# Performance work log

Measured on AMD Instinct MI355X. Metric: run time of the kernel, lower is better.

## Reference

```python
import jax, jax.numpy as jnp
import numpy as np

R = 0.15          # ball-query radius (module init arg r)
K = 32            # _MAX_NEIGHBOURS
B, N = 8, 4096


def _ball_query(pos, r, k):
    """Dense ball query. pos: [B,N,3] -> neighbor idx [B,N,K], sorted by distance.
    Slots with fewer than k in-radius neighbors are filled with the query's own
    index (self is always the first neighbor at distance 0), so their
    contribution to (f_i - f_j)^2 is exactly 0 -- matching torch-points-kernels'
    fill-with-first-neighbor behaviour."""
    d2 = jnp.sum((pos[:, :, None, :] - pos[:, None, :, :]) ** 2, axis=-1)  # [B,N,N]
    masked = jnp.where(d2 <= r * r, d2, jnp.inf)
    neg_vals, idx = jax.lax.top_k(-masked, k)          # ascending distance
    valid = neg_vals > -jnp.inf
    self_idx = jnp.arange(pos.shape[1])[None, :, None]
    return jnp.where(valid, idx, self_idx)             # [B,N,K]


def setup_inputs() -> dict:
    key = jax.random.key(0)
    k1, k2 = jax.random.split(key)
    pos = jax.random.uniform(k1, (B, N, 3), dtype=jnp.float32)
    f = jax.random.normal(k2, (B, N), dtype=jnp.float32)
    return {"pos": pos, "f": f}


def reference(pos, f):
    # neighbor indices are non-differentiable (torch gathers with long indices)
    nei_idx = jax.lax.stop_gradient(_ball_query(pos, R, K))      # [B,N,K]
    f_nei = jax.vmap(lambda fb, ib: fb[ib])(f, nei_idx)          # [B,N,K]
    variances = jnp.sum((f[:, :, None] - f_nei) ** 2, axis=-1)   # [B,N]
    return 0.5 * jnp.mean(variances)
```

## Files before the change

### kernel.cpp

```cpp
#include <hip/hip_runtime.h>


#define BQ_K 32
#define CAP 128
#define WPB 4
#define G 6
#define NC (G * G * G)
#define CAPC 512
#define QMAX 64
#define NPTS 4096
#define NPART 64
#define PSTRIDE 16

__device__ __forceinline__ int cell_coord(float x) {
    int c = (int)(x * (float)G);
    return c < 0 ? 0 : (c > G - 1 ? G - 1 : c);
}

__device__ __forceinline__ unsigned int decode_cnt(unsigned int v) {
    return (v >= 0x80000000u) ? (v - 0xAAAAAAAAu) : v;
}

__device__ __forceinline__ float select_sum(float2 e0, float2 e1, int M,
                                            float r2) {
    if (M <= BQ_K) return e0.y + e1.y;
    float lo = 0.0f, hi = r2 * 1.000001f;
    #pragma unroll
    for (int it = 0; it < 12; ++it) {
        const float mid = 0.5f * (lo + hi);
        const int cnt = __popcll(__ballot(e0.x < mid)) +
                        __popcll(__ballot(e1.x < mid));
        if (cnt >= BQ_K) hi = mid; else lo = mid;
    }
    float s = 0.0f;
    if (e0.x < hi) s = e0.y;
    if (e1.x < hi) s += e1.y;
    return s;
}

__device__ __forceinline__ float dual_select_sum(
    float2 a0, float2 a1, int MA, float2 b0, float2 b1, int MB, float r2)
{
    const bool needA = MA > BQ_K;
    const bool needB = MB > BQ_K;
    float hiA = 1e31f, hiB = 1e31f;
    if (needA || needB) {
        float loA = 0.0f, loB = 0.0f;
        if (needA) hiA = r2 * 1.000001f;
        if (needB) hiB = r2 * 1.000001f;
        const bool bigA = MA > 64, bigB = MB > 64;
        #pragma unroll
        for (int it = 0; it < 12; ++it) {
            if (needA) {
                const float mid = 0.5f * (loA + hiA);
                int c = __popcll(__ballot(a0.x < mid));
                if (bigA) c += __popcll(__ballot(a1.x < mid));
                if (c >= BQ_K) hiA = mid; else loA = mid;
            }
            if (needB) {
                const float mid = 0.5f * (loB + hiB);
                int c = __popcll(__ballot(b0.x < mid));
                if (bigB) c += __popcll(__ballot(b1.x < mid));
                if (c >= BQ_K) hiB = mid; else loB = mid;
            }
        }
    }
    float s = 0.0f;
    if (a0.x < hiA) s += a0.y;
    if (a1.x < hiA) s += a1.y;
    if (b0.x < hiB) s += b0.y;
    if (b1.x < hiB) s += b1.y;
    return s;
}

__global__ __launch_bounds__(256) void dl_fused(
    const float* __restrict__ pos, const float* __restrict__ f,
    float* __restrict__ partial, unsigned int* __restrict__ c1,
    unsigned int* __restrict__ c2, float* __restrict__ out,
    float r2, float scale)
{
    __shared__ float4 s_cand[CAPC];
    __shared__ float2 s_sel[WPB][2][CAP];
    __shared__ int    s_q[QMAX];
    __shared__ int    s_ncand, s_nq;
    __shared__ float  s_wsum[WPB];
    __shared__ int    s_last;

    const int bc = blockIdx.x;
    const int b  = bc / NC;
    const int c  = bc - b * NC;
    const int cx = c % G, cy = (c / G) % G, cz = c / (G * G);

    const int lane = threadIdx.x & 63;
    const int wave = threadIdx.x >> 6;
    const unsigned long long lmask = (1ULL << lane) - 1ULL;

    if (threadIdx.x == 0) { s_ncand = 0; s_nq = 0; s_last = 0; }
    __syncthreads();

    const float* posb = pos + (size_t)b * NPTS * 3;
    const float* fb   = f   + (size_t)b * NPTS;

    const float lox = cx * (1.0f / G), hix = lox + (1.0f / G);
    const float loy = cy * (1.0f / G), hiy = loy + (1.0f / G);
    const float loz = cz * (1.0f / G), hiz = loz + (1.0f / G);

    constexpr int per = NPTS / WPB;
    const int wbeg = wave * per;
    for (int j0 = 0; j0 < per; j0 += 64) {
        const int j = wbeg + j0 + lane;
        const float x  = posb[3 * j + 0];
        const float y  = posb[3 * j + 1];
        const float z  = posb[3 * j + 2];
        const float fv = fb[j];
        const float ddx = fmaxf(fmaxf(lox - x, x - hix), 0.0f);
        const float ddy = fmaxf(fmaxf(loy - y, y - hiy), 0.0f);
        const float ddz = fmaxf(fmaxf(loz - z, z - hiz), 0.0f);
        const float d2c = fmaf(ddx, ddx, fmaf(ddy, ddy, ddz * ddz));
        const bool in = (d2c <= r2);
        const unsigned long long m = __ballot(in);
        const int nh = __popcll(m);
        int base = 0;
        if (lane == 0 && nh) base = atomicAdd(&s_ncand, nh);
        base = __shfl(base, 0, 64);
        if (in) {
            const int off = base + __popcll(m & lmask);
            if (off < CAPC) {
                s_cand[off] = make_float4(x, y, z, fv);
                if (cell_coord(x) == cx && cell_coord(y) == cy &&
                    cell_coord(z) == cz) {
                    const int qs = atomicAdd(&s_nq, 1);
                    if (qs < QMAX) s_q[qs] = off;
                }
            }
        }
    }
    __syncthreads();

    const int ncand = s_ncand < CAPC ? s_ncand : CAPC;
    const int nq    = s_nq < QMAX ? s_nq : QMAX;
    const int ncB   = (ncand + 63) & ~63;

    for (int i = ncand + threadIdx.x; i < ncB; i += 256)
        s_cand[i] = make_float4(1e30f, 1e30f, 1e30f, 0.0f);
    __syncthreads();

    float2* selA = s_sel[wave][0];
    float2* selB = s_sel[wave][1];
    float wsum = 0.0f;

    for (int qi = wave; qi < nq; qi += 2 * WPB) {
        const int  qj    = qi + WPB;
        const bool haveB = qj < nq;
        const float4 qpA = s_cand[s_q[qi]];
        const float4 qpB = s_cand[s_q[haveB ? qj : qi]];
        const float qxA = qpA.x, qyA = qpA.y, qzA = qpA.z, fiA = qpA.w;
        const float qxB = qpB.x, qyB = qpB.y, qzB = qpB.z, fiB = qpB.w;

        int cinA = 0, cinB = 0;
        for (int basej = 0; basej < ncB; basej += 64) {
            const float4 cd = s_cand[basej + lane];
            const float dxA = cd.x - qxA, dyA = cd.y - qyA, dzA = cd.z - qzA;
            const float dxB = cd.x - qxB, dyB = cd.y - qyB, dzB = cd.z - qzB;
            const float d2A = fmaf(dxA, dxA, fmaf(dyA, dyA, dzA * dzA));
            const float d2B = fmaf(dxB, dxB, fmaf(dyB, dyB, dzB * dzB));
            const bool inbA = d2A <= r2;
            const bool inbB = haveB && (d2B <= r2);
            const unsigned long long mA = __ballot(inbA);
            const unsigned long long mB = __ballot(inbB);
            const int offA = cinA + __popcll(mA & lmask);
            const int offB = cinB + __popcll(mB & lmask);
            if (inbA && offA < CAP) {
                const float fd = fiA - cd.w;
                selA[offA] = make_float2(d2A, fd * fd);
            }
            if (inbB && offB < CAP) {
                const float fd = fiB - cd.w;
                selB[offB] = make_float2(d2B, fd * fd);
            }
            cinA += __popcll(mA);
            cinB += __popcll(mB);
        }
        const int MA = cinA < CAP ? cinA : CAP;
        const int MB = cinB < CAP ? cinB : CAP;
        const float2 a0 = (lane < MA) ? selA[lane] : make_float2(1e30f, 0.0f);
        const float2 a1 = (64 + lane < MA) ? selA[64 + lane]
                                           : make_float2(1e30f, 0.0f);
        const float2 b0 = (lane < MB) ? selB[lane] : make_float2(1e30f, 0.0f);
        const float2 b1 = (64 + lane < MB) ? selB[64 + lane]
                                           : make_float2(1e30f, 0.0f);
        wsum += dual_select_sum(a0, a1, MA, b0, b1, MB, r2);
    }

    for (int o = 32; o > 0; o >>= 1) wsum += __shfl_down(wsum, o, 64);
    if (lane == 0) s_wsum[wave] = wsum;
    __syncthreads();
    if (threadIdx.x == 0) {
        const float bs = s_wsum[0] + s_wsum[1] + s_wsum[2] + s_wsum[3];
        const int k = blockIdx.x & (NPART - 1);
        const float oldp = atomicAdd(&partial[k * PSTRIDE], bs);
        asm volatile("" :: "v"(oldp));
        const unsigned int expect = (gridDim.x - 1u - (unsigned)k) / 64u + 1u;
        const unsigned int oc =
            decode_cnt(atomicAdd(&c1[k * PSTRIDE], 1u));
        if (oc + 1u == expect) {
            const unsigned int o2 = decode_cnt(atomicAdd(c2, 1u));
            if (o2 + 1u == (unsigned)NPART)
                s_last = 1;
        }
    }
    __syncthreads();
    if (s_last && wave == 0) {
        float v = atomicAdd(&partial[lane * PSTRIDE], 0.0f);
        for (int o = 32; o > 0; o >>= 1) v += __shfl_down(v, o, 64);
        if (lane == 0) out[0] = v * scale;
    }
}

__global__ __launch_bounds__(256) void dl_fallback(
    const float* __restrict__ pos, const float* __restrict__ f,
    float* __restrict__ out, float r2, float scale)
{
    __shared__ float4 s_cand[CAPC];
    __shared__ float2 s_sel[WPB][CAP];
    __shared__ int    s_q[QMAX];
    __shared__ int    s_ncand, s_nq;
    __shared__ float  s_wsum[WPB];

    const int bc = blockIdx.x;
    const int b  = bc / NC;
    const int c  = bc - b * NC;
    const int cx = c % G, cy = (c / G) % G, cz = c / (G * G);
    const int lane = threadIdx.x & 63;
    const int wave = threadIdx.x >> 6;
    const unsigned long long lmask = (1ULL << lane) - 1ULL;

    if (threadIdx.x == 0) { s_ncand = 0; s_nq = 0; }
    __syncthreads();

    const float* posb = pos + (size_t)b * NPTS * 3;
    const float* fb   = f   + (size_t)b * NPTS;
    const float lox = cx * (1.0f / G), hix = lox + (1.0f / G);
    const float loy = cy * (1.0f / G), hiy = loy + (1.0f / G);
    const float loz = cz * (1.0f / G), hiz = loz + (1.0f / G);

    constexpr int per = NPTS / WPB;
    const int wbeg = wave * per;
    for (int j0 = 0; j0 < per; j0 += 64) {
        const int j = wbeg + j0 + lane;
        const float x  = posb[3 * j + 0];
        const float y  = posb[3 * j + 1];
        const float z  = posb[3 * j + 2];
        const float ddx = fmaxf(fmaxf(lox - x, x - hix), 0.0f);
        const float ddy = fmaxf(fmaxf(loy - y, y - hiy), 0.0f);
        const float ddz = fmaxf(fmaxf(loz - z, z - hiz), 0.0f);
        const float d2c = fmaf(ddx, ddx, fmaf(ddy, ddy, ddz * ddz));
        const bool in = (d2c <= r2);
        const unsigned long long m = __ballot(in);
        const int nh = __popcll(m);
        int base = 0;
        if (lane == 0 && nh) base = atomicAdd(&s_ncand, nh);
        base = __shfl(base, 0, 64);
        if (in) {
            const int off = base + __popcll(m & lmask);
            if (off < CAPC) {
                s_cand[off] = make_float4(x, y, z, fb[j]);
                if (cell_coord(x) == cx && cell_coord(y) == cy &&
                    cell_coord(z) == cz) {
                    const int qs = atomicAdd(&s_nq, 1);
                    if (qs < QMAX) s_q[qs] = off;
                }
            }
        }
    }
    __syncthreads();

    const int ncand = s_ncand < CAPC ? s_ncand : CAPC;
    const int nq    = s_nq < QMAX ? s_nq : QMAX;
    const int ncB   = (ncand + 63) & ~63;
    float2* sel = s_sel[wave];
    float wsum = 0.0f;

    for (int qi = wave; qi < nq; qi += WPB) {
        const float4 qp = s_cand[s_q[qi]];
        const float qx = qp.x, qy = qp.y, qz = qp.z, fi = qp.w;
        int cin = 0;
        for (int basej = 0; basej < ncB; basej += 64) {
            const float4 cd = s_cand[basej + lane];
            const bool valid = (basej + lane) < ncand;
            const float dx = cd.x - qx, dy = cd.y - qy, dz = cd.z - qz;
            const float d2 = fmaf(dx, dx, fmaf(dy, dy, dz * dz));
            const bool inb = valid && (d2 <= r2);
            const unsigned long long mm = __ballot(inb);
            const int off = cin + __popcll(mm & lmask);
            if (inb && off < CAP) {
                const float fd = fi - cd.w;
                sel[off] = make_float2(d2, fd * fd);
            }
            cin += __popcll(mm);
        }
        const int M = cin < CAP ? cin : CAP;
        const float2 e0 = (lane < M) ? sel[lane] : make_float2(1e30f, 0.0f);
        const float2 e1 = (64 + lane < M) ? sel[64 + lane]
                                          : make_float2(1e30f, 0.0f);
        wsum += select_sum(e0, e1, M, r2);
    }

    for (int o = 32; o > 0; o >>= 1) wsum += __shfl_down(wsum, o, 64);
    if (lane == 0) s_wsum[wave] = wsum;
    __syncthreads();
    if (threadIdx.x == 0) {
        const float bs = s_wsum[0] + s_wsum[1] + s_wsum[2] + s_wsum[3];
        atomicAdd(out, bs * scale);
    }
}

extern "C" void kernel_launch(void* const* d_in, const int* in_sizes, int n_in,
                              void* d_out, int out_size, void* d_ws, size_t ws_size,
                              hipStream_t stream) {
    const float* pos = (const float*)d_in[0];
    const float* f   = (const float*)d_in[1];
    float* out = (float*)d_out;

    const int B = in_sizes[1] / NPTS;
    const int total = B * NPTS;
    const float r2 = 0.15f * 0.15f;
    const float scale = 0.5f / (float)total;

    const size_t part_bytes = (size_t)NPART * PSTRIDE * sizeof(float);
    const size_t c1_bytes   = (size_t)NPART * PSTRIDE * sizeof(unsigned);
    const size_t c2_bytes   = 64;
    if (ws_size < part_bytes + c1_bytes + c2_bytes) {
        hipMemsetAsync(out, 0, sizeof(float), stream);
        dl_fallback<<<B * NC, 256, 0, stream>>>(pos, f, out, r2, scale);
        return;
    }

    char* wsp = (char*)d_ws;
    float*        partial = (float*)wsp;
    unsigned int* c1      = (unsigned int*)(wsp + part_bytes);
    unsigned int* c2      = (unsigned int*)(wsp + part_bytes + c1_bytes);

    dl_fused<<<B * NC, 256, 0, stream>>>(pos, f, partial, c1, c2, out,
                                         r2, scale);
}
```

Baseline: 79.48 us.

## Process two adjacent x-cells per block to share the point scan

Each block now handles a pair of neighbouring grid cells along x, scanning all points of the batch once and building two candidate lists and query lists in shared memory. Waves are split two per cell for the distance/selection phase. This halves the number of blocks and the redundant global reads of the full point set per cell, at the cost of doubled shared memory for candidates and half the waves per cell's query work.

```diff
diff --git a/kernel.cpp b/kernel.cpp
--- a/kernel.cpp
+++ b/kernel.cpp
@@ -6,6 +6,7 @@
 #define WPB 4
 #define G 6
 #define NC (G * G * G)
+#define NPAIR (NC / 2)
 #define CAPC 512
 #define QMAX 64
 #define NPTS 4096
@@ -73,35 +74,38 @@
     return s;
 }
 
-__global__ __launch_bounds__(256) void dl_fused(
+__global__ __launch_bounds__(256) void dl_fused2(
     const float* __restrict__ pos, const float* __restrict__ f,
     float* __restrict__ partial, unsigned int* __restrict__ c1,
     unsigned int* __restrict__ c2, float* __restrict__ out,
     float r2, float scale)
 {
-    __shared__ float4 s_cand[CAPC];
+    __shared__ float4 s_cand[2][CAPC];
     __shared__ float2 s_sel[WPB][2][CAP];
-    __shared__ int    s_q[QMAX];
-    __shared__ int    s_ncand, s_nq;
+    __shared__ int    s_q[2][QMAX];
+    __shared__ int    s_nc0, s_nc1, s_nq0, s_nq1;
     __shared__ float  s_wsum[WPB];
     __shared__ int    s_last;
 
     const int bc = blockIdx.x;
-    const int b  = bc / NC;
-    const int c  = bc - b * NC;
-    const int cx = c % G, cy = (c / G) % G, cz = c / (G * G);
+    const int b  = bc / NPAIR;
+    const int pr = bc - b * NPAIR;
+    const int c0 = pr * 2;
+    const int cx0 = c0 % G, cy = (c0 / G) % G, cz = c0 / (G * G);
 
     const int lane = threadIdx.x & 63;
     const int wave = threadIdx.x >> 6;
     const unsigned long long lmask = (1ULL << lane) - 1ULL;
 
-    if (threadIdx.x == 0) { s_ncand = 0; s_nq = 0; s_last = 0; }
+    if (threadIdx.x == 0) { s_nc0 = 0; s_nc1 = 0; s_nq0 = 0; s_nq1 = 0;
+                            s_last = 0; }
     __syncthreads();
 
     const float* posb = pos + (size_t)b * NPTS * 3;
     const float* fb   = f   + (size_t)b * NPTS;
 
-    const float lox = cx * (1.0f / G), hix = lox + (1.0f / G);
+    const float lox0 = cx0 * (1.0f / G), hix0 = lox0 + (1.0f / G);
+    const float hix1 = hix0 + (1.0f / G);
     const float loy = cy * (1.0f / G), hiy = loy + (1.0f / G);
     const float loz = cz * (1.0f / G), hiz = loz + (1.0f / G);
 
@@ -113,53 +117,90 @@
         const float y  = posb[3 * j + 1];
         const float z  = posb[3 * j + 2];
         const float fv = fb[j];
-        const float ddx = fmaxf(fmaxf(lox - x, x - hix), 0.0f);
         const float ddy = fmaxf(fmaxf(loy - y, y - hiy), 0.0f);
         const float ddz = fmaxf(fmaxf(loz - z, z - hiz), 0.0f);
-        const float d2c = fmaf(ddx, ddx, fmaf(ddy, ddy, ddz * ddz));
-        const bool in = (d2c <= r2);
-        const unsigned long long m = __ballot(in);
-        const int nh = __popcll(m);
-        int base = 0;
-        if (lane == 0 && nh) base = atomicAdd(&s_ncand, nh);
-        base = __shfl(base, 0, 64);
-        if (in) {
-            const int off = base + __popcll(m & lmask);
-            if (off < CAPC) {
-                s_cand[off] = make_float4(x, y, z, fv);
-                if (cell_coord(x) == cx && cell_coord(y) == cy &&
-                    cell_coord(z) == cz) {
-                    const int qs = atomicAdd(&s_nq, 1);
-                    if (qs < QMAX) s_q[qs] = off;
+        const float dyz2 = fmaf(ddy, ddy, ddz * ddz);
+        const float ddx0 = fmaxf(fmaxf(lox0 - x, x - hix0), 0.0f);
+        const float ddx1 = fmaxf(fmaxf(hix0 - x, x - hix1), 0.0f);
+        const float d20 = fmaf(ddx0, ddx0, dyz2);
+        const float d21 = fmaf(ddx1, ddx1, dyz2);
+        const bool in0 = d20 <= r2;
+        const bool in1 = d21 <= r2;
+        const bool yzq = (cell_coord(y) == cy) && (cell_coord(z) == cz);
+        const int  ccx = cell_coord(x);
+
+        {
+            const unsigned long long m = __ballot(in0);
+            const int nh = __popcll(m);
+            int base = 0;
+            if (lane == 0 && nh) base = atomicAdd(&s_nc0, nh);
+            base = __shfl(base, 0, 64);
+            if (in0) {
+                const int off = base + __popcll(m & lmask);
+                if (off < CAPC) {
+                    s_cand[0][off] = make_float4(x, y, z, fv);
+                    if (yzq && ccx == cx0) {
+                        const int qs = atomicAdd(&s_nq0, 1);
+                        if (qs < QMAX) s_q[0][qs] = off;
+                    }
                 }
             }
         }
-    }
-    __syncthreads();
-
-    const int ncand = s_ncand < CAPC ? s_ncand : CAPC;
-    const int nq    = s_nq < QMAX ? s_nq : QMAX;
-    const int ncB   = (ncand + 63) & ~63;
-
-    for (int i = ncand + threadIdx.x; i < ncB; i += 256)
-        s_cand[i] = make_float4(1e30f, 1e30f, 1e30f, 0.0f);
-    __syncthreads();
+        {
+            const unsigned long long m = __ballot(in1);
+            const int nh = __popcll(m);
+            int base = 0;
+            if (lane == 0 && nh) base = atomicAdd(&s_nc1, nh);
+            base = __shfl(base, 0, 64);
+            if (in1) {
+                const int off = base + __popcll(m & lmask);
+                if (off < CAPC) {
+                    s_cand[1][off] = make_float4(x, y, z, fv);
+                    if (yzq && ccx == cx0 + 1) {
+                        const int qs = atomicAdd(&s_nq1, 1);
+                        if (qs < QMAX) s_q[1][qs] = off;
+                    }
+                }
+            }
+        }
+    }
+    __syncthreads();
+
+    const int nc0 = s_nc0 < CAPC ? s_nc0 : CAPC;
+    const int nc1 = s_nc1 < CAPC ? s_nc1 : CAPC;
+    const int nq0 = s_nq0 < QMAX ? s_nq0 : QMAX;
+    const int nq1 = s_nq1 < QMAX ? s_nq1 : QMAX;
+    const int ncB0 = (nc0 + 63) & ~63;
+    const int ncB1 = (nc1 + 63) & ~63;
+
+    for (int i = nc0 + threadIdx.x; i < ncB0; i += 256)
+        s_cand[0][i] = make_float4(1e30f, 1e30f, 1e30f, 0.0f);
+    for (int i = nc1 + threadIdx.x; i < ncB1; i += 256)
+        s_cand[1][i] = make_float4(1e30f, 1e30f, 1e30f, 0.0f);
+    __syncthreads();
+
+    const int csel = wave >> 1;
+    const int wp   = wave & 1;
+    const float4* cand = s_cand[csel];
+    const int* qlist = s_q[csel];
+    const int nqc = csel ? nq1 : nq0;
+    const int ncBc = csel ? ncB1 : ncB0;
 
     float2* selA = s_sel[wave][0];
     float2* selB = s_sel[wave][1];
     float wsum = 0.0f;
 
-    for (int qi = wave; qi < nq; qi += 2 * WPB) {
-        const int  qj    = qi + WPB;
-        const bool haveB = qj < nq;
-        const float4 qpA = s_cand[s_q[qi]];
-        const float4 qpB = s_cand[s_q[haveB ? qj : qi]];
+    for (int qi = 2 * wp; qi < nqc; qi += 4) {
+        const int  qj    = qi + 1;
+        const bool haveB = qj < nqc;
+        const float4 qpA = cand[qlist[qi]];
+        const float4 qpB = cand[qlist[haveB ? qj : qi]];
         const float qxA = qpA.x, qyA = qpA.y, qzA = qpA.z, fiA = qpA.w;
         const float qxB = qpB.x, qyB = qpB.y, qzB = qpB.z, fiB = qpB.w;
 
         int cinA = 0, cinB = 0;
-        for (int basej = 0; basej < ncB; basej += 64) {
-            const float4 cd = s_cand[basej + lane];
+        for (int basej = 0; basej < ncBc; basej += 64) {
+            const float4 cd = cand[basej + lane];
             const float dxA = cd.x - qxA, dyA = cd.y - qyA, dzA = cd.z - qzA;
             const float dxB = cd.x - qxB, dyB = cd.y - qyB, dzB = cd.z - qzB;
             const float d2A = fmaf(dxA, dxA, fmaf(dyA, dyA, dzA * dzA));
@@ -341,6 +382,6 @@
     unsigned int* c1      = (unsigned int*)(wsp + part_bytes);
     unsigned int* c2      = (unsigned int*)(wsp + part_bytes + c1_bytes);
 
-    dl_fused<<<B * NC, 256, 0, stream>>>(pos, f, partial, c1, c2, out,
-                                         r2, scale);
-}
+    dl_fused2<<<B * NPAIR, 256, 0, stream>>>(pos, f, partial, c1, c2, out,
+                                             r2, scale);
+}
```

Result: slower. 90.01 us (+13.2%).

## Use 8 waves per block with 2x-unrolled candidate gather and paired queries

Applied to the files above, without the earlier changes.

The fused kernel now runs 512 threads (8 waves) per cell block instead of 256. Each wave scans half as many points, and the scan loop handles two 64-point chunks per iteration so the global loads can overlap. Each wave also takes adjacent query pairs. The fallback kernel is pinned to 4 waves. The aim is more latency hiding in the gather phase and more parallel query processing, at the cost of more shared memory per block and possibly fewer resident blocks, plus idle waves when a cell has few queries.

```diff
diff --git a/kernel.cpp b/kernel.cpp
--- a/kernel.cpp
+++ b/kernel.cpp
@@ -3,7 +3,7 @@
 
 #define BQ_K 32
 #define CAP 128
-#define WPB 4
+#define WPB 8
 #define G 6
 #define NC (G * G * G)
 #define CAPC 512
@@ -73,7 +73,7 @@
     return s;
 }
 
-__global__ __launch_bounds__(256) void dl_fused(
+__global__ __launch_bounds__(512, 8) void dl_fused8(
     const float* __restrict__ pos, const float* __restrict__ f,
     float* __restrict__ partial, unsigned int* __restrict__ c1,
     unsigned int* __restrict__ c2, float* __restrict__ out,
@@ -107,33 +107,58 @@
 
     constexpr int per = NPTS / WPB;
     const int wbeg = wave * per;
-    for (int j0 = 0; j0 < per; j0 += 64) {
-        const int j = wbeg + j0 + lane;
-        const float x  = posb[3 * j + 0];
-        const float y  = posb[3 * j + 1];
-        const float z  = posb[3 * j + 2];
-        const float fv = fb[j];
-        const float ddx = fmaxf(fmaxf(lox - x, x - hix), 0.0f);
-        const float ddy = fmaxf(fmaxf(loy - y, y - hiy), 0.0f);
-        const float ddz = fmaxf(fmaxf(loz - z, z - hiz), 0.0f);
-        const float d2c = fmaf(ddx, ddx, fmaf(ddy, ddy, ddz * ddz));
-        const bool in = (d2c <= r2);
-        const unsigned long long m = __ballot(in);
-        const int nh = __popcll(m);
+    for (int j0 = 0; j0 < per; j0 += 128) {
+        const int ja = wbeg + j0 + lane;
+        const int jb = ja + 64;
+        const float xa = posb[3 * ja + 0];
+        const float ya = posb[3 * ja + 1];
+        const float za = posb[3 * ja + 2];
+        const float fa = fb[ja];
+        const float xb = posb[3 * jb + 0];
+        const float yb = posb[3 * jb + 1];
+        const float zb = posb[3 * jb + 2];
+        const float fvb = fb[jb];
+
+        const float dax = fmaxf(fmaxf(lox - xa, xa - hix), 0.0f);
+        const float day = fmaxf(fmaxf(loy - ya, ya - hiy), 0.0f);
+        const float daz = fmaxf(fmaxf(loz - za, za - hiz), 0.0f);
+        const float d2a = fmaf(dax, dax, fmaf(day, day, daz * daz));
+        const float dbx = fmaxf(fmaxf(lox - xb, xb - hix), 0.0f);
+        const float dby = fmaxf(fmaxf(loy - yb, yb - hiy), 0.0f);
+        const float dbz = fmaxf(fmaxf(loz - zb, zb - hiz), 0.0f);
+        const float d2b = fmaf(dbx, dbx, fmaf(dby, dby, dbz * dbz));
+        const bool ina = d2a <= r2;
+        const bool inb = d2b <= r2;
+
+        const unsigned long long ma = __ballot(ina);
+        const unsigned long long mb = __ballot(inb);
+        const int na = __popcll(ma);
+        const int nh = na + __popcll(mb);
         int base = 0;
         if (lane == 0 && nh) base = atomicAdd(&s_ncand, nh);
         base = __shfl(base, 0, 64);
-        if (in) {
-            const int off = base + __popcll(m & lmask);
+        if (ina) {
+            const int off = base + __popcll(ma & lmask);
             if (off < CAPC) {
-                s_cand[off] = make_float4(x, y, z, fv);
-                if (cell_coord(x) == cx && cell_coord(y) == cy &&
-                    cell_coord(z) == cz) {
+                s_cand[off] = make_float4(xa, ya, za, fa);
+                if (cell_coord(xa) == cx && cell_coord(ya) == cy &&
+                    cell_coord(za) == cz) {
                     const int qs = atomicAdd(&s_nq, 1);
                     if (qs < QMAX) s_q[qs] = off;
                 }
             }
         }
+        if (inb) {
+            const int off = base + na + __popcll(mb & lmask);
+            if (off < CAPC) {
+                s_cand[off] = make_float4(xb, yb, zb, fvb);
+                if (cell_coord(xb) == cx && cell_coord(yb) == cy &&
+                    cell_coord(zb) == cz) {
+                    const int qs = atomicAdd(&s_nq, 1);
+                    if (qs < QMAX) s_q[qs] = off;
+                }
+            }
+        }
     }
     __syncthreads();
 
@@ -141,7 +166,7 @@
     const int nq    = s_nq < QMAX ? s_nq : QMAX;
     const int ncB   = (ncand + 63) & ~63;
 
-    for (int i = ncand + threadIdx.x; i < ncB; i += 256)
+    for (int i = ncand + threadIdx.x; i < ncB; i += 512)
         s_cand[i] = make_float4(1e30f, 1e30f, 1e30f, 0.0f);
     __syncthreads();
 
@@ -149,8 +174,8 @@
     float2* selB = s_sel[wave][1];
     float wsum = 0.0f;
 
-    for (int qi = wave; qi < nq; qi += 2 * WPB) {
-        const int  qj    = qi + WPB;
+    for (int qi = 2 * wave; qi < nq; qi += 2 * WPB) {
+        const int  qj    = qi + 1;
         const bool haveB = qj < nq;
         const float4 qpA = s_cand[s_q[qi]];
         const float4 qpB = s_cand[s_q[haveB ? qj : qi]];
@@ -196,7 +221,9 @@
     if (lane == 0) s_wsum[wave] = wsum;
     __syncthreads();
     if (threadIdx.x == 0) {
-        const float bs = s_wsum[0] + s_wsum[1] + s_wsum[2] + s_wsum[3];
+        float bs = 0.0f;
+        #pragma unroll
+        for (int w = 0; w < WPB; ++w) bs += s_wsum[w];
         const int k = blockIdx.x & (NPART - 1);
         const float oldp = atomicAdd(&partial[k * PSTRIDE], bs);
         asm volatile("" :: "v"(oldp));
@@ -222,10 +249,10 @@
     float* __restrict__ out, float r2, float scale)
 {
     __shared__ float4 s_cand[CAPC];
-    __shared__ float2 s_sel[WPB][CAP];
+    __shared__ float2 s_sel[4][CAP];
     __shared__ int    s_q[QMAX];
     __shared__ int    s_ncand, s_nq;
-    __shared__ float  s_wsum[WPB];
+    __shared__ float  s_wsum[4];
 
     const int bc = blockIdx.x;
     const int b  = bc / NC;
@@ -244,7 +271,7 @@
     const float loy = cy * (1.0f / G), hiy = loy + (1.0f / G);
     const float loz = cz * (1.0f / G), hiz = loz + (1.0f / G);
 
-    constexpr int per = NPTS / WPB;
+    constexpr int per = NPTS / 4;
     const int wbeg = wave * per;
     for (int j0 = 0; j0 < per; j0 += 64) {
         const int j = wbeg + j0 + lane;
@@ -281,7 +308,7 @@
     float2* sel = s_sel[wave];
     float wsum = 0.0f;
 
-    for (int qi = wave; qi < nq; qi += WPB) {
+    for (int qi = wave; qi < nq; qi += 4) {
         const float4 qp = s_cand[s_q[qi]];
         const float qx = qp.x, qy = qp.y, qz = qp.z, fi = qp.w;
         int cin = 0;
@@ -341,6 +368,6 @@
     unsigned int* c1      = (unsigned int*)(wsp + part_bytes);
     unsigned int* c2      = (unsigned int*)(wsp + part_bytes + c1_bytes);
 
-    dl_fused<<<B * NC, 256, 0, stream>>>(pos, f, partial, c1, c2, out,
-                                         r2, scale);
-}
+    dl_fused8<<<B * NC, 512, 0, stream>>>(pos, f, partial, c1, c2, out,
+                                          r2, scale);
+}
```

Result: faster. 77.41 us, median of 2 (-2.6%).
